# Performance work log

Hardware: AMD Instinct MI355X
Metric: run time of the kernel (lower is better)

The kernel has to match this reference:

```python
import jax, jax.numpy as jnp
import numpy as np

H = 32  # hidden_size
D = 512  # input_size


def _lstm_layer(x_tbd, Wih, Whh, b):
    """Single PyTorch-convention LSTM layer.
    x_tbd: [T, B, Din]; Wih: [4H, Din]; Whh: [4H, H]; b: [4H] (b_ih + b_hh).
    Gate order (PyTorch): i, f, g, o. Returns outputs [T, B, H]."""
    T, B, _ = x_tbd.shape
    # Precompute the input contribution for all timesteps at once.
    xg = jnp.einsum('tbd,gd->tbg', x_tbd, Wih) + b  # [T, B, 4H]

    def step(carry, xg_t):
        h, c = carry
        gates = xg_t + h @ Whh.T  # [B, 4H]
        i, f, g, o = jnp.split(gates, 4, axis=-1)
        i = jax.nn.sigmoid(i)
        f = jax.nn.sigmoid(f)
        g = jnp.tanh(g)
        o = jax.nn.sigmoid(o)
        c = f * c + i * g
        h = o * jnp.tanh(c)
        return (h, c), h

    h0 = jnp.zeros((B, H), dtype=x_tbd.dtype)
    c0 = jnp.zeros((B, H), dtype=x_tbd.dtype)
    _, ys = jax.lax.scan(step, (h0, c0), xg)
    return ys  # [T, B, H]


def setup_inputs() -> dict:
    key = jax.random.key(0)
    ks = jax.random.split(key, 9)
    s = 1.0 / np.sqrt(H)  # PyTorch LSTM init: U(-1/sqrt(H), 1/sqrt(H))
    u = lambda k, shape: jax.random.uniform(k, shape, jnp.float32, -s, s)
    return {
        'x': jax.random.normal(ks[0], (64, 1024, D), dtype=jnp.float32),
        'Wih0': u(ks[1], (4 * H, D)),
        'Whh0': u(ks[2], (4 * H, H)),
        'bih0': u(ks[3], (4 * H,)),
        'bhh0': u(ks[4], (4 * H,)),
        'Wih1': u(ks[5], (4 * H, H)),
        'Whh1': u(ks[6], (4 * H, H)),
        'bih1': u(ks[7], (4 * H,)),
        'bhh1': u(ks[8], (4 * H,)),
    }


def reference(x, Wih0, Whh0, bih0, bhh0, Wih1, Whh1, bih1, bhh1):
    # x: [B, T, D] (batch_first) -> scan over time axis
    x_tbd = jnp.transpose(x, (1, 0, 2))  # [T, B, D]
    y0 = _lstm_layer(x_tbd, Wih0, Whh0, bih0 + bhh0)  # [T, B, H]
    y1 = _lstm_layer(y0, Wih1, Whh1, bih1 + bhh1)     # [T, B, H]
    return jnp.transpose(y1, (1, 0, 2))  # [B, T, H]
```

## Files before the change

kernel.cpp:

```cpp
#include <hip/hip_runtime.h>
#include <stdint.h>


#define TT 1024
#define BB 64
#define DD 512
#define HH 32
#define GG 128

typedef _Float16 h2v __attribute__((ext_vector_type(2)));
typedef __fp16 pk2 __attribute__((ext_vector_type(2)));
typedef int int2v __attribute__((ext_vector_type(2)));
typedef _Float16 f16x8 __attribute__((ext_vector_type(8)));
typedef float f32x4 __attribute__((ext_vector_type(4)));

__device__ __forceinline__ uint32_t pack2(float lo, float hi) {
  pk2 p = __builtin_amdgcn_cvt_pkrtz(lo, hi);
  return __builtin_bit_cast(uint32_t, p);
}
__device__ __forceinline__ float dot2(uint32_t a, uint32_t b, float acc) {
  return __builtin_amdgcn_fdot2(__builtin_bit_cast(h2v, a),
                                __builtin_bit_cast(h2v, b), acc, false);
}
__device__ __forceinline__ float fast_rcp(float x) { return __builtin_amdgcn_rcpf(x); }
__device__ __forceinline__ float sigm(float s) { return fast_rcp(1.f + __expf(-s)); }
__device__ __forceinline__ float fast_tanh(float x) {
  return fmaf(2.f, fast_rcp(1.f + __expf(-2.f * x)), -1.f);
}
__device__ __forceinline__ float act_sel(float s, bool ist) {
  float z = ist ? s + s : s;
  float r = fast_rcp(1.f + __expf(-z));
  return ist ? fmaf(2.f, r, -1.f) : r;
}

__device__ __forceinline__ float partner32(float x) {
  int xi = __builtin_bit_cast(int, x);
#if __has_builtin(__builtin_amdgcn_permlane32_swap)
  int2v r = __builtin_amdgcn_permlane32_swap(xi, xi, false, false);
  return __builtin_bit_cast(float, r.x ^ r.y ^ xi);
#else
  int a = xi, b = xi;
  asm("v_permlane32_swap_b32 %0, %1" : "+v"(a), "+v"(b));
  return __builtin_bit_cast(float, a ^ b ^ xi);
#endif
}

__device__ __forceinline__ float xor1_dpp(float x) {
  int xi = __builtin_bit_cast(int, x);
  int r = __builtin_amdgcn_update_dpp(xi, xi, 0xB1, 0xF, 0xF, true);
  return __builtin_bit_cast(float, r);
}

__global__ __launch_bounds__(256) void xg_gemm_mfma(const float* __restrict__ x,
                                                    const float* __restrict__ W,
                                                    const float* __restrict__ bih,
                                                    const float* __restrict__ bhh,
                                                    float* __restrict__ outp) {
  __shared__ _Float16 lxs[128][40];
  __shared__ _Float16 lws[128][40];
  const int tid = threadIdx.x;
  const int m0 = blockIdx.x * 128;
  const int sr = tid >> 1;
  const int sk = (tid & 1) * 16;
  const int w = tid >> 6;
  const int wm = (w >> 1) * 64;
  const int wn = (w & 1) * 64;
  const int lane = tid & 63;
  const int lr = lane & 15;
  const int lk = (lane >> 4) * 8;

  f32x4 acc[4][4];
#pragma unroll
  for (int i = 0; i < 4; ++i)
#pragma unroll
    for (int j = 0; j < 4; ++j) acc[i][j] = (f32x4){0.f, 0.f, 0.f, 0.f};

  for (int k0 = 0; k0 < DD; k0 += 32) {
#pragma unroll
    for (int c = 0; c < 4; ++c) {
      const float4 xv = *(const float4*)(x + (size_t)(m0 + sr) * DD + k0 + sk + c * 4);
      uint2 px;
      px.x = pack2(xv.x, xv.y);
      px.y = pack2(xv.z, xv.w);
      *(uint2*)&lxs[sr][sk + c * 4] = px;
      const float4 wv = *(const float4*)(W + (size_t)sr * DD + k0 + sk + c * 4);
      uint2 pw;
      pw.x = pack2(wv.x, wv.y);
      pw.y = pack2(wv.z, wv.w);
      *(uint2*)&lws[sr][sk + c * 4] = pw;
    }
    __syncthreads();
    f16x8 af[4], bf[4];
#pragma unroll
    for (int s = 0; s < 4; ++s) {
      af[s] = *(const f16x8*)&lxs[wm + s * 16 + lr][lk];
      bf[s] = *(const f16x8*)&lws[wn + s * 16 + lr][lk];
    }
#pragma unroll
    for (int mi = 0; mi < 4; ++mi)
#pragma unroll
      for (int ni = 0; ni < 4; ++ni)
        acc[mi][ni] = __builtin_amdgcn_mfma_f32_16x16x32_f16(af[mi], bf[ni],
                                                             acc[mi][ni], 0, 0, 0);
    __syncthreads();
  }
  const int rq = (lane >> 4) * 4;
#pragma unroll
  for (int ni = 0; ni < 4; ++ni) {
    const int g = wn + ni * 16 + lr;
    const float bsum = bih[g] + bhh[g];
#pragma unroll
    for (int mi = 0; mi < 4; ++mi) {
      const int mbase = m0 + wm + mi * 16 + rq;
#pragma unroll
      for (int q = 0; q < 4; ++q)
        outp[(size_t)(mbase + q) * GG + g] = acc[mi][ni][q] + bsum;
    }
  }
}

__device__ __forceinline__ void load16(const uint32_t* p, uint32_t* v) {
  uint4 r0 = ((const uint4*)p)[0];
  uint4 r1 = ((const uint4*)p)[1];
  uint4 r2 = ((const uint4*)p)[2];
  uint4 r3 = ((const uint4*)p)[3];
  v[0] = r0.x; v[1] = r0.y; v[2] = r0.z; v[3] = r0.w;
  v[4] = r1.x; v[5] = r1.y; v[6] = r1.z; v[7] = r1.w;
  v[8] = r2.x; v[9] = r2.y; v[10] = r2.z; v[11] = r2.w;
  v[12] = r3.x; v[13] = r3.y; v[14] = r3.z; v[15] = r3.w;
}

__global__ __launch_bounds__(192)
void lstm_scan_sys(const float* __restrict__ xg,
                   const float* __restrict__ Whh0,
                   const float* __restrict__ Wih1,
                   const float* __restrict__ Whh1,
                   const float* __restrict__ bih1,
                   const float* __restrict__ bhh1,
                   float* __restrict__ out) {
  __shared__ alignas(16) uint32_t H0R[4][16];
  __shared__ alignas(16) uint32_t H1R[4][16];
  __shared__ alignas(16) float PIA[4][64];
  __shared__ alignas(16) float PIB[4][64];

  const int tid = threadIdx.x;
  const int wid = tid >> 6;
  const int l = tid & 63;
  const int j = l & 31;
  const int hi = l >> 5;
  const int b = blockIdx.x;
  const int gA = j + 64 * hi;
  const int gB = gA + 32;
  const bool wrt = (!hi) && ((j & 1) == 0);

  if (tid < 64) {
    H0R[tid >> 4][tid & 15] = 0u;
    H1R[tid >> 4][tid & 15] = 0u;
  }
  __syncthreads();

  uint32_t wA[16], wB[16];
  float b1A = 0.f, b1B = 0.f;
  float cc = 0.f;
  const float* xgp = xg + (size_t)b * TT * GG;
  float* outp = out + (size_t)b * TT * HH;
  float xA[4], xB[4];

  if (wid == 0) {
#pragma unroll
    for (int q = 0; q < 8; ++q) {
      float4 a = *(const float4*)(Whh0 + (size_t)gA * HH + q * 4);
      float4 c = *(const float4*)(Whh0 + (size_t)gB * HH + q * 4);
      wA[2 * q] = pack2(a.x, a.y); wA[2 * q + 1] = pack2(a.z, a.w);
      wB[2 * q] = pack2(c.x, c.y); wB[2 * q + 1] = pack2(c.z, c.w);
    }
#pragma unroll
    for (int u = 0; u < 4; ++u) {
      xA[u] = xgp[u * GG + gA];
      xB[u] = xgp[u * GG + gB];
    }
  } else if (wid == 1) {
#pragma unroll
    for (int q = 0; q < 8; ++q) {
      float4 d = *(const float4*)(Wih1 + (size_t)gA * HH + q * 4);
      float4 e = *(const float4*)(Wih1 + (size_t)gB * HH + q * 4);
      wA[2 * q] = pack2(d.x, d.y); wA[2 * q + 1] = pack2(d.z, d.w);
      wB[2 * q] = pack2(e.x, e.y); wB[2 * q + 1] = pack2(e.z, e.w);
    }
    b1A = bih1[gA] + bhh1[gA];
    b1B = bih1[gB] + bhh1[gB];
  } else {
#pragma unroll
    for (int q = 0; q < 8; ++q) {
      float4 f = *(const float4*)(Whh1 + (size_t)gA * HH + q * 4);
      float4 g = *(const float4*)(Whh1 + (size_t)gB * HH + q * 4);
      wA[2 * q] = pack2(f.x, f.y); wA[2 * q + 1] = pack2(f.z, f.w);
      wB[2 * q] = pack2(g.x, g.y); wB[2 * q + 1] = pack2(g.z, g.w);
    }
  }

  for (int s = 0; s < TT + 2; ++s) {
    if (wid == 0) {
      if (s < TT) {
        uint32_t h0v[16];
        load16(&H0R[(s - 1) & 3][0], h0v);
        float sA0 = xA[s & 3], sB0 = xB[s & 3];
        const int tp = (s + 4 < TT) ? (s + 4) : (TT - 1);
        xA[s & 3] = xgp[(size_t)tp * GG + gA];
        xB[s & 3] = xgp[(size_t)tp * GG + gB];
        float pA = 0.f, pB = 0.f;
#pragma unroll
        for (int k = 0; k < 16; k += 2) {
          sA0 = dot2(wA[k], h0v[k], sA0);
          pA  = dot2(wA[k + 1], h0v[k + 1], pA);
          sB0 = dot2(wB[k], h0v[k], sB0);
          pB  = dot2(wB[k + 1], h0v[k + 1], pB);
        }
        sA0 += pA; sB0 += pB;
        float aA = act_sel(sA0, hi != 0);
        float aB = sigm(sB0);
        float pAx = partner32(aA);
        float pBx = partner32(aB);
        float gi = hi ? pAx : aA;
        float gf = hi ? pBx : aB;
        float gg = hi ? aA : pAx;
        float go = hi ? aB : pBx;
        cc = fmaf(gf, cc, gi * gg);
        float h = go * fast_tanh(cc);
        float oth = xor1_dpp(h);
        float lo = (j & 1) ? oth : h;
        float hh = (j & 1) ? h : oth;
        uint32_t pk = pack2(lo, hh);
        if (wrt) H0R[s & 3][j >> 1] = pk;
      }
    } else if (wid == 1) {
      if (s >= 1 && s <= TT) {
        const int tau = s - 1;
        uint32_t h0v[16];
        load16(&H0R[tau & 3][0], h0v);
        float a0 = b1A, a1 = 0.f, b0 = b1B, b1v = 0.f;
#pragma unroll
        for (int k = 0; k < 16; k += 2) {
          a0 = dot2(wA[k], h0v[k], a0);
          a1 = dot2(wA[k + 1], h0v[k + 1], a1);
          b0 = dot2(wB[k], h0v[k], b0);
          b1v = dot2(wB[k + 1], h0v[k + 1], b1v);
        }
        PIA[tau & 3][l] = a0 + a1;
        PIB[tau & 3][l] = b0 + b1v;
      }
    } else {
      if (s >= 2) {
        const int tau = s - 2;
        uint32_t h1v[16];
        load16(&H1R[(tau - 1) & 3][0], h1v);
        float sA1 = PIA[tau & 3][l];
        float sB1 = PIB[tau & 3][l];
        float qA = 0.f, qB = 0.f;
#pragma unroll
        for (int k = 0; k < 16; k += 2) {
          sA1 = dot2(wA[k], h1v[k], sA1);
          qA  = dot2(wA[k + 1], h1v[k + 1], qA);
          sB1 = dot2(wB[k], h1v[k], sB1);
          qB  = dot2(wB[k + 1], h1v[k + 1], qB);
        }
        sA1 += qA; sB1 += qB;
        float aA = act_sel(sA1, hi != 0);
        float aB = sigm(sB1);
        float pAx = partner32(aA);
        float pBx = partner32(aB);
        float gi = hi ? pAx : aA;
        float gf = hi ? pBx : aB;
        float gg = hi ? aA : pAx;
        float go = hi ? aB : pBx;
        cc = fmaf(gf, cc, gi * gg);
        float h = go * fast_tanh(cc);
        if (!hi) outp[(size_t)tau * HH + j] = h;
        float oth = xor1_dpp(h);
        float lo = (j & 1) ? oth : h;
        float hh = (j & 1) ? h : oth;
        uint32_t pk = pack2(lo, hh);
        if (wrt) H1R[tau & 3][j >> 1] = pk;
      }
    }
    __syncthreads();
  }
}

extern "C" void kernel_launch(void* const* d_in, const int* in_sizes, int n_in,
                              void* d_out, int out_size, void* d_ws, size_t ws_size,
                              hipStream_t stream) {
  const float* x = (const float*)d_in[0];
  const float* Wih0 = (const float*)d_in[1];
  const float* Whh0 = (const float*)d_in[2];
  const float* bih0 = (const float*)d_in[3];
  const float* bhh0 = (const float*)d_in[4];
  const float* Wih1 = (const float*)d_in[5];
  const float* Whh1 = (const float*)d_in[6];
  const float* bih1 = (const float*)d_in[7];
  const float* bhh1 = (const float*)d_in[8];
  float* out = (float*)d_out;
  float* xg = (float*)d_ws;

  xg_gemm_mfma<<<dim3((BB * TT) / 128), dim3(256), 0, stream>>>(x, Wih0, bih0, bhh0, xg);
  lstm_scan_sys<<<dim3(BB), dim3(192), 0, stream>>>(xg, Whh0, Wih1, Whh1, bih1, bhh1, out);
}
```

Before: 410.8 us.

## Keep recurrent hidden state in registers via readlane and process two steps per barrier

Each layer's recurrent wave now broadcasts its packed hidden state into registers with readlane instead of reading it back from shared memory. The pipelined loop processes two timesteps per iteration, so the number of block-wide barriers is halved. The ring buffers still separate the slots used by producer and consumer. The trade-off is 16 readlane instructions per step and a longer per-phase critical path, since layer 1 now lags layer 0 by four steps.

```diff
diff --git a/kernel.cpp b/kernel.cpp
--- a/kernel.cpp
+++ b/kernel.cpp
@@ -131,15 +131,14 @@
 }
 
 __global__ __launch_bounds__(192)
-void lstm_scan_sys(const float* __restrict__ xg,
-                   const float* __restrict__ Whh0,
-                   const float* __restrict__ Wih1,
-                   const float* __restrict__ Whh1,
-                   const float* __restrict__ bih1,
-                   const float* __restrict__ bhh1,
-                   float* __restrict__ out) {
+void lstm_scan_sys2(const float* __restrict__ xg,
+                    const float* __restrict__ Whh0,
+                    const float* __restrict__ Wih1,
+                    const float* __restrict__ Whh1,
+                    const float* __restrict__ bih1,
+                    const float* __restrict__ bhh1,
+                    float* __restrict__ out) {
   __shared__ alignas(16) uint32_t H0R[4][16];
-  __shared__ alignas(16) uint32_t H1R[4][16];
   __shared__ alignas(16) float PIA[4][64];
   __shared__ alignas(16) float PIB[4][64];
 
@@ -153,15 +152,13 @@
   const int gB = gA + 32;
   const bool wrt = (!hi) && ((j & 1) == 0);
 
-  if (tid < 64) {
-    H0R[tid >> 4][tid & 15] = 0u;
-    H1R[tid >> 4][tid & 15] = 0u;
-  }
-  __syncthreads();
-
   uint32_t wA[16], wB[16];
   float b1A = 0.f, b1B = 0.f;
   float cc = 0.f;
+  uint32_t hreg[16];
+#pragma unroll
+  for (int k = 0; k < 16; ++k) hreg[k] = 0u;
+
   const float* xgp = xg + (size_t)b * TT * GG;
   float* outp = out + (size_t)b * TT * HH;
   float xA[4], xB[4];
@@ -198,89 +195,101 @@
       wB[2 * q] = pack2(g.x, g.y); wB[2 * q + 1] = pack2(g.z, g.w);
     }
   }
-
-  for (int s = 0; s < TT + 2; ++s) {
+  __syncthreads();
+
+  for (int p = 0; p <= TT / 2 + 1; ++p) {
     if (wid == 0) {
-      if (s < TT) {
-        uint32_t h0v[16];
-        load16(&H0R[(s - 1) & 3][0], h0v);
-        float sA0 = xA[s & 3], sB0 = xB[s & 3];
-        const int tp = (s + 4 < TT) ? (s + 4) : (TT - 1);
-        xA[s & 3] = xgp[(size_t)tp * GG + gA];
-        xB[s & 3] = xgp[(size_t)tp * GG + gB];
-        float pA = 0.f, pB = 0.f;
-#pragma unroll
-        for (int k = 0; k < 16; k += 2) {
-          sA0 = dot2(wA[k], h0v[k], sA0);
-          pA  = dot2(wA[k + 1], h0v[k + 1], pA);
-          sB0 = dot2(wB[k], h0v[k], sB0);
-          pB  = dot2(wB[k + 1], h0v[k + 1], pB);
+#pragma unroll
+      for (int u = 0; u < 2; ++u) {
+        const int s = 2 * p + u;
+        if (s < TT) {
+          float sA0 = xA[s & 3], sB0 = xB[s & 3];
+          const int tp = (s + 4 < TT) ? (s + 4) : (TT - 1);
+          xA[s & 3] = xgp[(size_t)tp * GG + gA];
+          xB[s & 3] = xgp[(size_t)tp * GG + gB];
+          float pA = 0.f, pB = 0.f;
+#pragma unroll
+          for (int k = 0; k < 16; k += 2) {
+            sA0 = dot2(wA[k], hreg[k], sA0);
+            pA  = dot2(wA[k + 1], hreg[k + 1], pA);
+            sB0 = dot2(wB[k], hreg[k], sB0);
+            pB  = dot2(wB[k + 1], hreg[k + 1], pB);
+          }
+          sA0 += pA; sB0 += pB;
+          float aA = act_sel(sA0, hi != 0);
+          float aB = sigm(sB0);
+          float pAx = partner32(aA);
+          float pBx = partner32(aB);
+          float gi = hi ? pAx : aA;
+          float gf = hi ? pBx : aB;
+          float gg = hi ? aA : pAx;
+          float go = hi ? aB : pBx;
+          cc = fmaf(gf, cc, gi * gg);
+          float h = go * fast_tanh(cc);
+          float oth = xor1_dpp(h);
+          float lo = (j & 1) ? oth : h;
+          float hh = (j & 1) ? h : oth;
+          uint32_t pk = pack2(lo, hh);
+          if (wrt) H0R[s & 3][j >> 1] = pk;
+#pragma unroll
+          for (int m = 0; m < 16; ++m)
+            hreg[m] = (uint32_t)__builtin_amdgcn_readlane((int)pk, 2 * m);
         }
-        sA0 += pA; sB0 += pB;
-        float aA = act_sel(sA0, hi != 0);
-        float aB = sigm(sB0);
-        float pAx = partner32(aA);
-        float pBx = partner32(aB);
-        float gi = hi ? pAx : aA;
-        float gf = hi ? pBx : aB;
-        float gg = hi ? aA : pAx;
-        float go = hi ? aB : pBx;
-        cc = fmaf(gf, cc, gi * gg);
-        float h = go * fast_tanh(cc);
-        float oth = xor1_dpp(h);
-        float lo = (j & 1) ? oth : h;
-        float hh = (j & 1) ? h : oth;
-        uint32_t pk = pack2(lo, hh);
-        if (wrt) H0R[s & 3][j >> 1] = pk;
       }
     } else if (wid == 1) {
-      if (s >= 1 && s <= TT) {
-        const int tau = s - 1;
-        uint32_t h0v[16];
-        load16(&H0R[tau & 3][0], h0v);
-        float a0 = b1A, a1 = 0.f, b0 = b1B, b1v = 0.f;
-#pragma unroll
-        for (int k = 0; k < 16; k += 2) {
-          a0 = dot2(wA[k], h0v[k], a0);
-          a1 = dot2(wA[k + 1], h0v[k + 1], a1);
-          b0 = dot2(wB[k], h0v[k], b0);
-          b1v = dot2(wB[k + 1], h0v[k + 1], b1v);
+#pragma unroll
+      for (int u = 0; u < 2; ++u) {
+        const int tau = 2 * p - 2 + u;
+        if (tau >= 0 && tau < TT) {
+          uint32_t h0v[16];
+          load16(&H0R[tau & 3][0], h0v);
+          float a0 = b1A, a1 = 0.f, b0 = b1B, b1v = 0.f;
+#pragma unroll
+          for (int k = 0; k < 16; k += 2) {
+            a0 = dot2(wA[k], h0v[k], a0);
+            a1 = dot2(wA[k + 1], h0v[k + 1], a1);
+            b0 = dot2(wB[k], h0v[k], b0);
+            b1v = dot2(wB[k + 1], h0v[k + 1], b1v);
+          }
+          PIA[tau & 3][l] = a0 + a1;
+          PIB[tau & 3][l] = b0 + b1v;
         }
-        PIA[tau & 3][l] = a0 + a1;
-        PIB[tau & 3][l] = b0 + b1v;
       }
     } else {
-      if (s >= 2) {
-        const int tau = s - 2;
-        uint32_t h1v[16];
-        load16(&H1R[(tau - 1) & 3][0], h1v);
-        float sA1 = PIA[tau & 3][l];
-        float sB1 = PIB[tau & 3][l];
-        float qA = 0.f, qB = 0.f;
-#pragma unroll
-        for (int k = 0; k < 16; k += 2) {
-          sA1 = dot2(wA[k], h1v[k], sA1);
-          qA  = dot2(wA[k + 1], h1v[k + 1], qA);
-          sB1 = dot2(wB[k], h1v[k], sB1);
-          qB  = dot2(wB[k + 1], h1v[k + 1], qB);
+#pragma unroll
+      for (int u = 0; u < 2; ++u) {
+        const int tau = 2 * p - 4 + u;
+        if (tau >= 0 && tau < TT) {
+          float sA1 = PIA[tau & 3][l];
+          float sB1 = PIB[tau & 3][l];
+          float qA = 0.f, qB = 0.f;
+#pragma unroll
+          for (int k = 0; k < 16; k += 2) {
+            sA1 = dot2(wA[k], hreg[k], sA1);
+            qA  = dot2(wA[k + 1], hreg[k + 1], qA);
+            sB1 = dot2(wB[k], hreg[k], sB1);
+            qB  = dot2(wB[k + 1], hreg[k + 1], qB);
+          }
+          sA1 += qA; sB1 += qB;
+          float aA = act_sel(sA1, hi != 0);
+          float aB = sigm(sB1);
+          float pAx = partner32(aA);
+          float pBx = partner32(aB);
+          float gi = hi ? pAx : aA;
+          float gf = hi ? pBx : aB;
+          float gg = hi ? aA : pAx;
+          float go = hi ? aB : pBx;
+          cc = fmaf(gf, cc, gi * gg);
+          float h = go * fast_tanh(cc);
+          if (!hi) outp[(size_t)tau * HH + j] = h;
+          float oth = xor1_dpp(h);
+          float lo = (j & 1) ? oth : h;
+          float hh = (j & 1) ? h : oth;
+          uint32_t pk = pack2(lo, hh);
+#pragma unroll
+          for (int m = 0; m < 16; ++m)
+            hreg[m] = (uint32_t)__builtin_amdgcn_readlane((int)pk, 2 * m);
         }
-        sA1 += qA; sB1 += qB;
-        float aA = act_sel(sA1, hi != 0);
-        float aB = sigm(sB1);
-        float pAx = partner32(aA);
-        float pBx = partner32(aB);
-        float gi = hi ? pAx : aA;
-        float gf = hi ? pBx : aB;
-        float gg = hi ? aA : pAx;
-        float go = hi ? aB : pBx;
-        cc = fmaf(gf, cc, gi * gg);
-        float h = go * fast_tanh(cc);
-        if (!hi) outp[(size_t)tau * HH + j] = h;
-        float oth = xor1_dpp(h);
-        float lo = (j & 1) ? oth : h;
-        float hh = (j & 1) ? h : oth;
-        uint32_t pk = pack2(lo, hh);
-        if (wrt) H1R[tau & 3][j >> 1] = pk;
       }
     }
     __syncthreads();
@@ -303,5 +312,5 @@
   float* xg = (float*)d_ws;
 
   xg_gemm_mfma<<<dim3((BB * TT) / 128), dim3(256), 0, stream>>>(x, Wih0, bih0, bhh0, xg);
-  lstm_scan_sys<<<dim3(BB), dim3(192), 0, stream>>>(xg, Whh0, Wih1, Whh1, bih1, bhh1, out);
-}
+  lstm_scan_sys2<<<dim3(BB), dim3(192), 0, stream>>>(xg, Whh0, Wih1, Whh1, bih1, bhh1, out);
+}
```

Measured after the change: 443.8 us. 8.0% more time.
